# Performance work log

Measured on AMD Instinct MI355X. Metric: run time of the kernel, lower is better.

The kernel has to match this reference:

```python
import jax, jax.numpy as jnp
import numpy as np

N = 1_000_000      # rows
D = 64             # input feature dim
INNER = 16         # inner_dim (Cholesky size)
OUT = 64           # out_dim (proj output)
NSEG = 100_000     # num_segments
NET_OUT = INNER * (INNER + 1) // 2 + INNER  # 152


def setup_inputs() -> dict:
    key = jax.random.key(0)
    k0, k1, k2, k3 = jax.random.split(key, 4)
    data = jax.random.normal(k0, (N, D), dtype=jnp.float32)
    segments = jax.random.randint(k1, (N,), 0, NSEG)
    # LazyInMLP([]) -> single Dense(net_out_dim) with kernel_init=normal(stddev=1e-2)
    W = jax.random.normal(k2, (D, NET_OUT), dtype=jnp.float32) * 0.01
    b = jnp.zeros((NET_OUT,), dtype=jnp.float32)
    # proj Dense(out_dim, use_bias=False), lecun-normal-ish scale
    proj_W = jax.random.normal(k3, (INNER, OUT), dtype=jnp.float32) * (1.0 / np.sqrt(INNER))
    return {"data": data, "segments": segments, "num_segments": NSEG,
            "W": W, "b": b, "proj_W": proj_W}


def reference(data, segments, num_segments, W, b, proj_W):
    # MLP (zero hidden layers -> single Dense)
    net_out = data @ W + b                      # [N, 152]
    t = net_out[:, :INNER]                      # [N, 16]
    y = net_out[:, INNER:]                      # [N, 136]

    # vectorized un_chol: fill lower triangle with tanh, then softplus the diag
    rows, cols = jnp.tril_indices(INNER)
    L = jnp.zeros((data.shape[0], INNER, INNER), dtype=data.dtype)
    L = L.at[:, rows, cols].set(jnp.tanh(y))
    di = jnp.arange(INNER)
    L = L.at[:, di, di].set(jax.nn.softplus(L[:, di, di]))
    F = jnp.einsum('nik,njk->nij', L, L)        # L @ L.T, [N, 16, 16]

    # segment reductions (reduction='sum')
    F_red = jax.ops.segment_sum(F, segments, num_segments=num_segments)  # [S,16,16]
    t_red = jax.ops.segment_sum(t, segments, num_segments=num_segments)  # [S,16]

    F_masked = F_red + jnp.eye(INNER, dtype=F_red.dtype)
    F_inv = jnp.linalg.inv(F_masked)            # batched small-matrix inverse
    # NOTE: faithful to source einsum '...ij,...j->...j' (sums over i, keeps j)
    theta = jnp.einsum('sij,sj->sj', F_inv, t_red)  # [S, 16]

    # inner_dim != out_dim -> proj Dense (no bias)
    return theta @ proj_W                       # [S, 64]
```

## Files before the change

### kernel.cpp

```cpp
#include <hip/hip_runtime.h>
#include <hip/hip_bf16.h>


#define N_PTS   1000000
#define DIM     64
#define INNER   16
#define OUTD    64
#define NSEG    100000
#define NTRI    136
#define NET_OUT 152
#define NB      391
#define SEGW    7
#define NWAVES  ((NSEG + SEGW - 1) / SEGW)
#define MAINB   ((NWAVES + 3) / 4)

typedef short bf16x8 __attribute__((ext_vector_type(8)));
typedef float f32x4  __attribute__((ext_vector_type(4)));
typedef float f32x2  __attribute__((ext_vector_type(2)));
typedef __bf16 bfv2  __attribute__((ext_vector_type(2)));

__device__ __host__ __forceinline__ constexpr int tri(int i) { return i * (i + 1) / 2; }

__device__ __forceinline__ float fast_tanh(float x) {
    float e = __expf(2.0f * x);
    return 1.0f - __fdividef(2.0f, e + 1.0f);
}
__device__ __forceinline__ float fast_softplus(float x) {
    return __logf(1.0f + __expf(x));
}
__device__ __forceinline__ unsigned short cvt1(float f) {
    __bf16 h = (__bf16)f;
    return __builtin_bit_cast(unsigned short, h);
}
__device__ __forceinline__ unsigned cvt2(float a, float b) {
    f32x2 t; t[0] = a; t[1] = b;
    bfv2 h = __builtin_convertvector(t, bfv2);
    return __builtin_bit_cast(unsigned, h);
}

__device__ __forceinline__ void wave_lds_sync() {
    __builtin_amdgcn_wave_barrier();
    __builtin_amdgcn_s_waitcnt(0xC07F);
    __builtin_amdgcn_wave_barrier();
}

__device__ __forceinline__ void ecoord(int e, int& r, int& c, bool& dg) {
    int rr = 0;
    #pragma unroll
    for (int k = 1; k < 16; ++k) rr = (e >= tri(k)) ? k : rr;
    r = rr; c = e - tri(rr); dg = (c == rr);
}

__global__ __launch_bounds__(256) void hist_kernel(const int* __restrict__ segs,
                                                   int* __restrict__ cnt,
                                                   int* __restrict__ rank)
{
    int t = blockIdx.x * 256 + threadIdx.x;
    if (t < N_PTS) rank[t] = atomicAdd(&cnt[segs[t]], 1);
}

__global__ __launch_bounds__(256) void scan_blocks(const int* __restrict__ cnt,
                                                   int* __restrict__ off,
                                                   int* __restrict__ bsum)
{
    __shared__ int sh[256];
    const int t = threadIdx.x;
    const int i = blockIdx.x * 256 + t;
    int v = (i < NSEG) ? cnt[i] : 0;
    sh[t] = v;
    __syncthreads();
    #pragma unroll
    for (int d = 1; d < 256; d <<= 1) {
        int add = (t >= d) ? sh[t - d] : 0;
        __syncthreads();
        sh[t] += add;
        __syncthreads();
    }
    if (i < NSEG) off[i] = sh[t] - v;
    if (t == 255) bsum[blockIdx.x] = sh[t];
}

__global__ __launch_bounds__(512) void scan_top(int* __restrict__ bsum)
{
    __shared__ int sh[512];
    const int t = threadIdx.x;
    int v = (t < NB) ? bsum[t] : 0;
    sh[t] = v;
    __syncthreads();
    #pragma unroll
    for (int d = 1; d < 512; d <<= 1) {
        int add = (t >= d) ? sh[t - d] : 0;
        __syncthreads();
        sh[t] += add;
        __syncthreads();
    }
    if (t < NB) bsum[t] = sh[t] - v;
}

__global__ __launch_bounds__(256) void scan_add(int* __restrict__ off,
                                                const int* __restrict__ bsum)
{
    int i = blockIdx.x * 256 + threadIdx.x;
    if (i < NSEG) off[i] += bsum[blockIdx.x];
}

__global__ __launch_bounds__(256) void scatter_kernel(const int* __restrict__ segs,
                                                      const int* __restrict__ off,
                                                      const int* __restrict__ rank,
                                                      int* __restrict__ sorted)
{
    int t = blockIdx.x * 256 + threadIdx.x;
    if (t < N_PTS) sorted[off[segs[t]] + rank[t]] = t;
}

__global__ __launch_bounds__(256, 2)
void main_kernel(const float* __restrict__ data,
                 const int*   __restrict__ sorted,
                 const int*   __restrict__ off,
                 const int*   __restrict__ cnt,
                 const float* __restrict__ W,
                 const float* __restrict__ bias,
                 float* __restrict__ Fred,
                 float* __restrict__ tred)
{
    __shared__ __align__(16) unsigned short lds[4 * 4096];
    const int l = threadIdx.x & 63;
    const int w = threadIdx.x >> 6;
    unsigned short* Lw = &lds[w * 4096];
    const int c = l & 15;
    const int q = l >> 4;

    const int wave_id = blockIdx.x * 4 + w;
    const int ws0 = wave_id * SEGW;
    if (ws0 >= NSEG) return;
    const int ws1 = min(ws0 + SEGW, NSEG);

    int Ek[SEGW];
    int gend = 0;
    #pragma unroll
    for (int k = 0; k < SEGW; ++k) {
        const int s = ws0 + k;
        if (s < ws1) { gend = off[s] + cnt[s]; Ek[k] = gend; }
        else           Ek[k] = 0x7fffffff;
    }
    int g = off[ws0];
    if (g >= gend) return;

    #pragma unroll
    for (int u = 0; u < 32; ++u) ((unsigned*)Lw)[u * 64 + l] = 0u;
    wave_lds_sync();

    bf16x8 wf[10][2];
    float  bT[10];
    #pragma unroll
    for (int T = 0; T < 10; ++T) {
        #pragma unroll
        for (int ks = 0; ks < 2; ++ks) {
            bf16x8 f;
            #pragma unroll
            for (int j = 0; j < 8; ++j) {
                int k = 32 * ks + 8 * q + j;
                int n = 16 * T + c;
                f[j] = (n < NET_OUT) ? (short)cvt1(W[k * NET_OUT + n]) : (short)0;
            }
            wf[T][ks] = f;
        }
        int n = 16 * T + c;
        bT[T] = (n < NET_OUT) ? bias[n] : 0.0f;
    }

    int rcoff[9];
    int dgmask = 0, dgoff0 = 0;
    #pragma unroll
    for (int T = 1; T <= 9; ++T) {
        int e = 16 * (T - 1) + c;
        int re, ce; bool dg;
        ecoord(e, re, ce, dg);
        rcoff[T - 1] = re * 16 + ce;
        if (dg && (T < 9 || c < 8)) {
            dgmask |= 1 << T;
            if (T <= 8) dgoff0 = re * 16 + ce;
        }
    }
    const bool v9     = (c < 8);
    const bool hasdg0 = (c != 15);
    const int  qb     = q << 10;

    f32x4 fa = {0.f, 0.f, 0.f, 0.f};
    f32x4 fb = {0.f, 0.f, 0.f, 0.f};
    float tcarry = 0.f;
    int a_start = 0;
    float dsv0 = 0.f, dsv1 = 0.f, dsv2 = 0.f, dsv3 = 0.f;

    const int lofs = c * 16 + (q & 1) * 8 + (q >> 1) * 256;

    int idx = min(g + c, gend - 1);
    int p   = sorted[idx];

    while (g < gend) {
        const int nv   = min(16, gend - g);
        const int gn   = g + nv;
        const int idxn = min(gn + c, gend - 1);
        const int pnx  = sorted[idxn];

        int segl = 0;
        bool flag = false;
        #pragma unroll
        for (int k = 0; k < SEGW; ++k) {
            segl += (idx >= Ek[k]) ? 1 : 0;
            flag |= (idx == Ek[k] - 1);
        }
        const int sidv = ws0 + segl;
        const unsigned long long bm = __ballot(l < 16 && c < nv && flag);

        bf16x8 af[2];
        #pragma unroll
        for (int ks = 0; ks < 2; ++ks) {
            const float4* dp = (const float4*)(data + (size_t)p * DIM + 32 * ks + 8 * q);
            float4 x0 = dp[0], x1 = dp[1];
            bf16x8 f;
            unsigned* fu = (unsigned*)&f;
            fu[0] = cvt2(x0.x, x0.y); fu[1] = cvt2(x0.z, x0.w);
            fu[2] = cvt2(x1.x, x1.y); fu[3] = cvt2(x1.z, x1.w);
            af[ks] = f;
        }

        f32x4 acc0;
        {
            f32x4 z = {0.f, 0.f, 0.f, 0.f};
            z = __builtin_amdgcn_mfma_f32_16x16x32_bf16(af[0], wf[0][0], z, 0, 0, 0);
            acc0 = __builtin_amdgcn_mfma_f32_16x16x32_bf16(af[1], wf[0][1], z, 0, 0, 0);
        }

        float s0 = acc0[0] + bT[0];
        float s1 = s0 + acc0[1] + bT[0];
        float s2 = s1 + acc0[2] + bT[0];
        float s3 = s2 + acc0[3] + bT[0];
        float u  = s3;
        float v16 = __shfl_up(u, 16, 64);
        float v32 = __shfl_up(u, 32, 64);
        float v48 = __shfl_up(u, 48, 64);
        float excl = (q >= 1 ? v16 : 0.f) + (q >= 2 ? v32 : 0.f) + (q >= 3 ? v48 : 0.f);
        float P0 = excl + s0, P1 = excl + s1, P2 = excl + s2, P3 = excl + s3;

        wave_lds_sync();
        #pragma unroll
        for (int T = 1; T <= 9; ++T) {
            f32x4 z = {0.f, 0.f, 0.f, 0.f};
            z = __builtin_amdgcn_mfma_f32_16x16x32_bf16(af[0], wf[T][0], z, 0, 0, 0);
            f32x4 a2 = __builtin_amdgcn_mfma_f32_16x16x32_bf16(af[1], wf[T][1], z, 0, 0, 0);
            const bool isdg = (dgmask >> T) & 1;
            const bool st   = (T < 9 || v9) && !isdg;
            unsigned short* bp = Lw + (qb + rcoff[T - 1]);
            #pragma unroll
            for (int r = 0; r < 4; ++r) {
                float v = fast_tanh(a2[r] + bT[T]);
                if (st) bp[r * 256] = cvt1(v);
                if (T <= 8) {
                    if (r == 0) dsv0 = isdg ? v : dsv0;
                    if (r == 1) dsv1 = isdg ? v : dsv1;
                    if (r == 2) dsv2 = isdg ? v : dsv2;
                    if (r == 3) dsv3 = isdg ? v : dsv3;
                }
            }
            if (T == 9 && (c == 7)) {
                unsigned short* dp9 = Lw + (qb + 255);
                #pragma unroll
                for (int r = 0; r < 4; ++r) {
                    float v = fast_tanh(a2[r] + bT[9]);
                    dp9[r * 256] = cvt1(fast_softplus(v));
                }
            }
        }
        if (hasdg0) {
            unsigned short* dp0 = Lw + (qb + dgoff0);
            dp0[0]   = cvt1(fast_softplus(dsv0));
            dp0[256] = cvt1(fast_softplus(dsv1));
            dp0[512] = cvt1(fast_softplus(dsv2));
            dp0[768] = cvt1(fast_softplus(dsv3));
        }
        wave_lds_sync();

        auto flush = [&](int i) {
            const int sid = __shfl(sidv, i, 64);
            const int rs = i & 3;
            float vi = (rs == 0) ? P0 : (rs == 1) ? P1 : (rs == 2) ? P2 : P3;
            float Pi = __shfl(vi, ((i >> 2) << 4) | c, 64);
            float Pe = 0.f;
            if (a_start > 0) {
                const int aa = a_start - 1, ra = aa & 3;
                float va = (ra == 0) ? P0 : (ra == 1) ? P1 : (ra == 2) ? P2 : P3;
                Pe = __shfl(va, ((aa >> 2) << 4) | c, 64);
            }
            float ts = Pi - Pe + tcarry;
            if (l < 16) tred[(size_t)sid * INNER + c] = ts;
            tcarry = 0.f;
            f32x4 ft = fa + fb;
            #pragma unroll
            for (int r = 0; r < 4; ++r) {
                const int mr = 4 * q + r;
                if (c <= mr)
                    Fred[(size_t)sid * NTRI + tri(mr) + c] = ft[r];
            }
            fa = (f32x4){0.f, 0.f, 0.f, 0.f};
            fb = (f32x4){0.f, 0.f, 0.f, 0.f};
            a_start = i + 1;
        };

        const int npair = (nv + 1) >> 1;
        for (int j = 0; j < npair; ++j) {
            const int i0 = 2 * j, i1 = i0 + 1;
            bf16x8 lf = *(const bf16x8*)(Lw + i0 * 256 + lofs);
            const bool vld1 = (i1 < nv);
            const bool f0 = (bm >> i0) & 1;
            if (vld1 && !f0) {
                if (j & 1) fb = __builtin_amdgcn_mfma_f32_16x16x32_bf16(lf, lf, fb, 0, 0, 0);
                else       fa = __builtin_amdgcn_mfma_f32_16x16x32_bf16(lf, lf, fa, 0, 0, 0);
                if ((bm >> i1) & 1) flush(i1);
            } else {
                const bf16x8 zz = {0, 0, 0, 0, 0, 0, 0, 0};
                bf16x8 lo = (q < 2) ? lf : zz;
                fa = __builtin_amdgcn_mfma_f32_16x16x32_bf16(lo, lo, fa, 0, 0, 0);
                if (f0) flush(i0);
                if (vld1) {
                    bf16x8 hi = (q >= 2) ? lf : zz;
                    fb = __builtin_amdgcn_mfma_f32_16x16x32_bf16(hi, hi, fb, 0, 0, 0);
                    if ((bm >> i1) & 1) flush(i1);
                }
            }
        }

        if (a_start < nv) {
            const int ii = nv - 1, rs = ii & 3;
            float vi = (rs == 0) ? P0 : (rs == 1) ? P1 : (rs == 2) ? P2 : P3;
            float Pi = __shfl(vi, ((ii >> 2) << 4) | c, 64);
            float Pe = 0.f;
            if (a_start > 0) {
                const int aa = a_start - 1, ra = aa & 3;
                float va = (ra == 0) ? P0 : (ra == 1) ? P1 : (ra == 2) ? P2 : P3;
                Pe = __shfl(va, ((aa >> 2) << 4) | c, 64);
            }
            tcarry += Pi - Pe;
        }
        a_start = 0;
        g = gn; idx = idxn; p = pnx;
    }
}

__global__ __launch_bounds__(256, 2)
void seg_kernel(const float* __restrict__ Fred,
                const float* __restrict__ tred,
                const int*   __restrict__ cnt,
                const float* __restrict__ projW,
                float* __restrict__ out)
{
    const int s = blockIdx.x * 256 + threadIdx.x;
    if (s >= NSEG) return;
    float* orow = out + (size_t)s * OUTD;

    if (cnt[s] == 0) {
        float4 zz = {0.f, 0.f, 0.f, 0.f};
        #pragma unroll
        for (int oc = 0; oc < OUTD; oc += 4) *(float4*)(orow + oc) = zz;
        return;
    }

    float a[NTRI];
    const float4* f4 = (const float4*)(Fred + (size_t)s * NTRI);
    #pragma unroll
    for (int qq = 0; qq < NTRI / 4; ++qq) {
        float4 v = f4[qq];
        a[4 * qq + 0] = v.x; a[4 * qq + 1] = v.y;
        a[4 * qq + 2] = v.z; a[4 * qq + 3] = v.w;
    }
    #pragma unroll
    for (int ii = 0; ii < INNER; ++ii) a[tri(ii) + ii] += 1.0f;

    #pragma unroll
    for (int j = 0; j < INNER; ++j) {
        float d = a[tri(j) + j];
        #pragma unroll
        for (int k = 0; k < j; ++k)
            d = fmaf(-a[tri(j) + k], a[tri(j) + k], d);
        d = sqrtf(d);
        a[tri(j) + j] = d;
        float dinv = __fdividef(1.0f, d);
        #pragma unroll
        for (int ii = j + 1; ii < INNER; ++ii) {
            float v = a[tri(ii) + j];
            #pragma unroll
            for (int k = 0; k < j; ++k)
                v = fmaf(-a[tri(ii) + k], a[tri(j) + k], v);
            a[tri(ii) + j] = v * dinv;
        }
    }
    float z[INNER];
    #pragma unroll
    for (int ii = 0; ii < INNER; ++ii) {
        float v = 1.0f;
        #pragma unroll
        for (int k = 0; k < ii; ++k)
            v = fmaf(-a[tri(ii) + k], z[k], v);
        z[ii] = __fdividef(v, a[tri(ii) + ii]);
    }
    float x[INNER];
    #pragma unroll
    for (int ii = INNER - 1; ii >= 0; --ii) {
        float v = z[ii];
        #pragma unroll
        for (int k = ii + 1; k < INNER; ++k)
            v = fmaf(-a[tri(k) + ii], x[k], v);
        x[ii] = __fdividef(v, a[tri(ii) + ii]);
    }
    float theta[INNER];
    const float4* t4 = (const float4*)(tred + (size_t)s * INNER);
    #pragma unroll
    for (int qq = 0; qq < 4; ++qq) {
        float4 v = t4[qq];
        theta[4 * qq + 0] = v.x * x[4 * qq + 0];
        theta[4 * qq + 1] = v.y * x[4 * qq + 1];
        theta[4 * qq + 2] = v.z * x[4 * qq + 2];
        theta[4 * qq + 3] = v.w * x[4 * qq + 3];
    }
    for (int oc = 0; oc < OUTD; oc += 8) {
        float acc[8] = {0, 0, 0, 0, 0, 0, 0, 0};
        #pragma unroll
        for (int j = 0; j < INNER; ++j) {
            float th = theta[j];
            #pragma unroll
            for (int uu = 0; uu < 8; ++uu)
                acc[uu] = fmaf(th, projW[j * OUTD + oc + uu], acc[uu]);
        }
        float4 v0 = {acc[0], acc[1], acc[2], acc[3]};
        float4 v1 = {acc[4], acc[5], acc[6], acc[7]};
        ((float4*)(orow + oc))[0] = v0;
        ((float4*)(orow + oc))[1] = v1;
    }
}

extern "C" void kernel_launch(void* const* d_in, const int* in_sizes, int n_in,
                              void* d_out, int out_size, void* d_ws, size_t ws_size,
                              hipStream_t stream)
{
    const float* data  = (const float*)d_in[0];
    const int*   segs  = (const int*)d_in[1];
    const float* W     = (const float*)d_in[3];
    const float* bias  = (const float*)d_in[4];
    const float* projW = (const float*)d_in[5];

    int* cnt     = (int*)d_ws;
    int* off     = cnt + NSEG;
    int* bsum    = off + NSEG;
    int* rank    = bsum + 512;
    int* sorted  = rank + N_PTS;
    float* Fred  = (float*)(sorted + N_PTS);
    float* tred  = Fred + (size_t)NSEG * NTRI;

    hipMemsetAsync(cnt, 0, NSEG * sizeof(int), stream);

    hist_kernel   <<<(N_PTS + 255) / 256, 256, 0, stream>>>(segs, cnt, rank);
    scan_blocks   <<<NB, 256, 0, stream>>>(cnt, off, bsum);
    scan_top      <<<1, 512, 0, stream>>>(bsum);
    scan_add      <<<NB, 256, 0, stream>>>(off, bsum);
    scatter_kernel<<<(N_PTS + 255) / 256, 256, 0, stream>>>(segs, off, rank, sorted);
    main_kernel   <<<MAINB, 256, 0, stream>>>(data, sorted, off, cnt, W, bias, Fred, tred);
    seg_kernel    <<<NB, 256, 0, stream>>>(Fred, tred, cnt, projW, (float*)d_out);
}
```

Baseline: 635.5 us.

## Make main kernel persistent with atomic work queue and prefetch next data rows

```diff
diff --git a/kernel.cpp b/kernel.cpp
--- a/kernel.cpp
+++ b/kernel.cpp
@@ -11,8 +11,7 @@
 #define NET_OUT 152
 #define NB      391
 #define SEGW    7
-#define NWAVES  ((NSEG + SEGW - 1) / SEGW)
-#define MAINB   ((NWAVES + 3) / 4)
+#define PERSB   1024
 
 typedef short bf16x8 __attribute__((ext_vector_type(8)));
 typedef float f32x4  __attribute__((ext_vector_type(4)));
@@ -121,7 +120,8 @@
                  const float* __restrict__ W,
                  const float* __restrict__ bias,
                  float* __restrict__ Fred,
-                 float* __restrict__ tred)
+                 float* __restrict__ tred,
+                 int*   __restrict__ wctr)
 {
     __shared__ __align__(16) unsigned short lds[4 * 4096];
     const int l = threadIdx.x & 63;
@@ -129,22 +129,6 @@
     unsigned short* Lw = &lds[w * 4096];
     const int c = l & 15;
     const int q = l >> 4;
-
-    const int wave_id = blockIdx.x * 4 + w;
-    const int ws0 = wave_id * SEGW;
-    if (ws0 >= NSEG) return;
-    const int ws1 = min(ws0 + SEGW, NSEG);
-
-    int Ek[SEGW];
-    int gend = 0;
-    #pragma unroll
-    for (int k = 0; k < SEGW; ++k) {
-        const int s = ws0 + k;
-        if (s < ws1) { gend = off[s] + cnt[s]; Ek[k] = gend; }
-        else           Ek[k] = 0x7fffffff;
-    }
-    int g = off[ws0];
-    if (g >= gend) return;
 
     #pragma unroll
     for (int u = 0; u < 32; ++u) ((unsigned*)Lw)[u * 64 + l] = 0u;
@@ -186,164 +170,197 @@
     const bool hasdg0 = (c != 15);
     const int  qb     = q << 10;
 
-    f32x4 fa = {0.f, 0.f, 0.f, 0.f};
-    f32x4 fb = {0.f, 0.f, 0.f, 0.f};
-    float tcarry = 0.f;
-    int a_start = 0;
-    float dsv0 = 0.f, dsv1 = 0.f, dsv2 = 0.f, dsv3 = 0.f;
-
     const int lofs = c * 16 + (q & 1) * 8 + (q >> 1) * 256;
 
-    int idx = min(g + c, gend - 1);
-    int p   = sorted[idx];
-
-    while (g < gend) {
-        const int nv   = min(16, gend - g);
-        const int gn   = g + nv;
-        const int idxn = min(gn + c, gend - 1);
-        const int pnx  = sorted[idxn];
-
-        int segl = 0;
-        bool flag = false;
+    for (;;) {
+        int base;
+        if (l == 0) base = atomicAdd(wctr, SEGW);
+        base = __shfl(base, 0, 64);
+        if (base >= NSEG) break;
+        const int ws0 = base;
+        const int ws1 = min(ws0 + SEGW, NSEG);
+
+        int Ek[SEGW];
+        int gend = 0;
         #pragma unroll
         for (int k = 0; k < SEGW; ++k) {
-            segl += (idx >= Ek[k]) ? 1 : 0;
-            flag |= (idx == Ek[k] - 1);
-        }
-        const int sidv = ws0 + segl;
-        const unsigned long long bm = __ballot(l < 16 && c < nv && flag);
-
-        bf16x8 af[2];
-        #pragma unroll
-        for (int ks = 0; ks < 2; ++ks) {
-            const float4* dp = (const float4*)(data + (size_t)p * DIM + 32 * ks + 8 * q);
-            float4 x0 = dp[0], x1 = dp[1];
-            bf16x8 f;
-            unsigned* fu = (unsigned*)&f;
-            fu[0] = cvt2(x0.x, x0.y); fu[1] = cvt2(x0.z, x0.w);
-            fu[2] = cvt2(x1.x, x1.y); fu[3] = cvt2(x1.z, x1.w);
-            af[ks] = f;
-        }
-
-        f32x4 acc0;
+            const int s = ws0 + k;
+            if (s < ws1) { gend = off[s] + cnt[s]; Ek[k] = gend; }
+            else           Ek[k] = 0x7fffffff;
+        }
+        int g = off[ws0];
+        if (g >= gend) continue;
+
+        f32x4 fa = {0.f, 0.f, 0.f, 0.f};
+        f32x4 fb = {0.f, 0.f, 0.f, 0.f};
+        float tcarry = 0.f;
+        int a_start = 0;
+        float dsv0 = 0.f, dsv1 = 0.f, dsv2 = 0.f, dsv3 = 0.f;
+
+        int idx = min(g + c, gend - 1);
         {
-            f32x4 z = {0.f, 0.f, 0.f, 0.f};
-            z = __builtin_amdgcn_mfma_f32_16x16x32_bf16(af[0], wf[0][0], z, 0, 0, 0);
-            acc0 = __builtin_amdgcn_mfma_f32_16x16x32_bf16(af[1], wf[0][1], z, 0, 0, 0);
-        }
-
-        float s0 = acc0[0] + bT[0];
-        float s1 = s0 + acc0[1] + bT[0];
-        float s2 = s1 + acc0[2] + bT[0];
-        float s3 = s2 + acc0[3] + bT[0];
-        float u  = s3;
-        float v16 = __shfl_up(u, 16, 64);
-        float v32 = __shfl_up(u, 32, 64);
-        float v48 = __shfl_up(u, 48, 64);
-        float excl = (q >= 1 ? v16 : 0.f) + (q >= 2 ? v32 : 0.f) + (q >= 3 ? v48 : 0.f);
-        float P0 = excl + s0, P1 = excl + s1, P2 = excl + s2, P3 = excl + s3;
-
-        wave_lds_sync();
-        #pragma unroll
-        for (int T = 1; T <= 9; ++T) {
-            f32x4 z = {0.f, 0.f, 0.f, 0.f};
-            z = __builtin_amdgcn_mfma_f32_16x16x32_bf16(af[0], wf[T][0], z, 0, 0, 0);
-            f32x4 a2 = __builtin_amdgcn_mfma_f32_16x16x32_bf16(af[1], wf[T][1], z, 0, 0, 0);
-            const bool isdg = (dgmask >> T) & 1;
-            const bool st   = (T < 9 || v9) && !isdg;
-            unsigned short* bp = Lw + (qb + rcoff[T - 1]);
-            #pragma unroll
-            for (int r = 0; r < 4; ++r) {
-                float v = fast_tanh(a2[r] + bT[T]);
-                if (st) bp[r * 256] = cvt1(v);
-                if (T <= 8) {
-                    if (r == 0) dsv0 = isdg ? v : dsv0;
-                    if (r == 1) dsv1 = isdg ? v : dsv1;
-                    if (r == 2) dsv2 = isdg ? v : dsv2;
-                    if (r == 3) dsv3 = isdg ? v : dsv3;
-                }
+            const int p0 = sorted[idx];
+            const float* dpt = data + (size_t)p0 * DIM + 8 * q;
+            float4 x0 = ((const float4*)dpt)[0];
+            float4 x1 = ((const float4*)dpt)[1];
+            float4 x2 = ((const float4*)(dpt + 32))[0];
+            float4 x3 = ((const float4*)(dpt + 32))[1];
+
+            while (g < gend) {
+                const int nv   = min(16, gend - g);
+                const int gn   = g + nv;
+                const int idxn = min(gn + c, gend - 1);
+                const int pnx  = sorted[idxn];
+                const float* dq = data + (size_t)pnx * DIM + 8 * q;
+                float4 y0 = ((const float4*)dq)[0];
+                float4 y1 = ((const float4*)dq)[1];
+                float4 y2 = ((const float4*)(dq + 32))[0];
+                float4 y3 = ((const float4*)(dq + 32))[1];
+
+                int segl = 0;
+                bool flag = false;
+                #pragma unroll
+                for (int k = 0; k < SEGW; ++k) {
+                    segl += (idx >= Ek[k]) ? 1 : 0;
+                    flag |= (idx == Ek[k] - 1);
+                }
+                const int sidv = ws0 + segl;
+                const unsigned long long bm = __ballot(l < 16 && c < nv && flag);
+
+                bf16x8 af[2];
+                {
+                    bf16x8 f;
+                    unsigned* fu = (unsigned*)&f;
+                    fu[0] = cvt2(x0.x, x0.y); fu[1] = cvt2(x0.z, x0.w);
+                    fu[2] = cvt2(x1.x, x1.y); fu[3] = cvt2(x1.z, x1.w);
+                    af[0] = f;
+                    fu[0] = cvt2(x2.x, x2.y); fu[1] = cvt2(x2.z, x2.w);
+                    fu[2] = cvt2(x3.x, x3.y); fu[3] = cvt2(x3.z, x3.w);
+                    af[1] = f;
+                }
+
+                f32x4 acc0;
+                {
+                    f32x4 z = {0.f, 0.f, 0.f, 0.f};
+                    z = __builtin_amdgcn_mfma_f32_16x16x32_bf16(af[0], wf[0][0], z, 0, 0, 0);
+                    acc0 = __builtin_amdgcn_mfma_f32_16x16x32_bf16(af[1], wf[0][1], z, 0, 0, 0);
+                }
+
+                float s0 = acc0[0] + bT[0];
+                float s1 = s0 + acc0[1] + bT[0];
+                float s2 = s1 + acc0[2] + bT[0];
+                float s3 = s2 + acc0[3] + bT[0];
+                float u  = s3;
+                float v16 = __shfl_up(u, 16, 64);
+                float v32 = __shfl_up(u, 32, 64);
+                float v48 = __shfl_up(u, 48, 64);
+                float excl = (q >= 1 ? v16 : 0.f) + (q >= 2 ? v32 : 0.f) + (q >= 3 ? v48 : 0.f);
+                float P0 = excl + s0, P1 = excl + s1, P2 = excl + s2, P3 = excl + s3;
+
+                wave_lds_sync();
+                #pragma unroll
+                for (int T = 1; T <= 9; ++T) {
+                    f32x4 z = {0.f, 0.f, 0.f, 0.f};
+                    z = __builtin_amdgcn_mfma_f32_16x16x32_bf16(af[0], wf[T][0], z, 0, 0, 0);
+                    f32x4 a2 = __builtin_amdgcn_mfma_f32_16x16x32_bf16(af[1], wf[T][1], z, 0, 0, 0);
+                    const bool isdg = (dgmask >> T) & 1;
+                    const bool st   = (T < 9 || v9) && !isdg;
+                    unsigned short* bp = Lw + (qb + rcoff[T - 1]);
+                    #pragma unroll
+                    for (int r = 0; r < 4; ++r) {
+                        float v = fast_tanh(a2[r] + bT[T]);
+                        if (st) bp[r * 256] = cvt1(v);
+                        if (T <= 8) {
+                            if (r == 0) dsv0 = isdg ? v : dsv0;
+                            if (r == 1) dsv1 = isdg ? v : dsv1;
+                            if (r == 2) dsv2 = isdg ? v : dsv2;
+                            if (r == 3) dsv3 = isdg ? v : dsv3;
+                        }
+                    }
+                    if (T == 9 && (c == 7)) {
+                        unsigned short* dp9 = Lw + (qb + 255);
+                        #pragma unroll
+                        for (int r = 0; r < 4; ++r) {
+                            float v = fast_tanh(a2[r] + bT[9]);
+                            dp9[r * 256] = cvt1(fast_softplus(v));
+                        }
+                    }
+                }
+                if (hasdg0) {
+                    unsigned short* dp0 = Lw + (qb + dgoff0);
+                    dp0[0]   = cvt1(fast_softplus(dsv0));
+                    dp0[256] = cvt1(fast_softplus(dsv1));
+                    dp0[512] = cvt1(fast_softplus(dsv2));
+                    dp0[768] = cvt1(fast_softplus(dsv3));
+                }
+                wave_lds_sync();
+
+                auto flush = [&](int i) {
+                    const int sid = __shfl(sidv, i, 64);
+                    const int rs = i & 3;
+                    float vi = (rs == 0) ? P0 : (rs == 1) ? P1 : (rs == 2) ? P2 : P3;
+                    float Pi = __shfl(vi, ((i >> 2) << 4) | c, 64);
+                    float Pe = 0.f;
+                    if (a_start > 0) {
+                        const int aa = a_start - 1, ra = aa & 3;
+                        float va = (ra == 0) ? P0 : (ra == 1) ? P1 : (ra == 2) ? P2 : P3;
+                        Pe = __shfl(va, ((aa >> 2) << 4) | c, 64);
+                    }
+                    float ts = Pi - Pe + tcarry;
+                    if (l < 16) tred[(size_t)sid * INNER + c] = ts;
+                    tcarry = 0.f;
+                    f32x4 ft = fa + fb;
+                    #pragma unroll
+                    for (int r = 0; r < 4; ++r) {
+                        const int mr = 4 * q + r;
+                        if (c <= mr)
+                            Fred[(size_t)sid * NTRI + tri(mr) + c] = ft[r];
+                    }
+                    fa = (f32x4){0.f, 0.f, 0.f, 0.f};
+                    fb = (f32x4){0.f, 0.f, 0.f, 0.f};
+                    a_start = i + 1;
+                };
+
+                const int npair = (nv + 1) >> 1;
+                for (int j = 0; j < npair; ++j) {
+                    const int i0 = 2 * j, i1 = i0 + 1;
+                    bf16x8 lf = *(const bf16x8*)(Lw + i0 * 256 + lofs);
+                    const bool vld1 = (i1 < nv);
+                    const bool f0 = (bm >> i0) & 1;
+                    if (vld1 && !f0) {
+                        if (j & 1) fb = __builtin_amdgcn_mfma_f32_16x16x32_bf16(lf, lf, fb, 0, 0, 0);
+                        else       fa = __builtin_amdgcn_mfma_f32_16x16x32_bf16(lf, lf, fa, 0, 0, 0);
+                        if ((bm >> i1) & 1) flush(i1);
+                    } else {
+                        const bf16x8 zz = {0, 0, 0, 0, 0, 0, 0, 0};
+                        bf16x8 lo = (q < 2) ? lf : zz;
+                        fa = __builtin_amdgcn_mfma_f32_16x16x32_bf16(lo, lo, fa, 0, 0, 0);
+                        if (f0) flush(i0);
+                        if (vld1) {
+                            bf16x8 hi = (q >= 2) ? lf : zz;
+                            fb = __builtin_amdgcn_mfma_f32_16x16x32_bf16(hi, hi, fb, 0, 0, 0);
+                            if ((bm >> i1) & 1) flush(i1);
+                        }
+                    }
+                }
+
+                if (a_start < nv) {
+                    const int ii = nv - 1, rs = ii & 3;
+                    float vi = (rs == 0) ? P0 : (rs == 1) ? P1 : (rs == 2) ? P2 : P3;
+                    float Pi = __shfl(vi, ((ii >> 2) << 4) | c, 64);
+                    float Pe = 0.f;
+                    if (a_start > 0) {
+                        const int aa = a_start - 1, ra = aa & 3;
+                        float va = (ra == 0) ? P0 : (ra == 1) ? P1 : (ra == 2) ? P2 : P3;
+                        Pe = __shfl(va, ((aa >> 2) << 4) | c, 64);
+                    }
+                    tcarry += Pi - Pe;
+                }
+                a_start = 0;
+                g = gn; idx = idxn;
+                x0 = y0; x1 = y1; x2 = y2; x3 = y3;
             }
-            if (T == 9 && (c == 7)) {
-                unsigned short* dp9 = Lw + (qb + 255);
-                #pragma unroll
-                for (int r = 0; r < 4; ++r) {
-                    float v = fast_tanh(a2[r] + bT[9]);
-                    dp9[r * 256] = cvt1(fast_softplus(v));
-                }
-            }
-        }
-        if (hasdg0) {
-            unsigned short* dp0 = Lw + (qb + dgoff0);
-            dp0[0]   = cvt1(fast_softplus(dsv0));
-            dp0[256] = cvt1(fast_softplus(dsv1));
-            dp0[512] = cvt1(fast_softplus(dsv2));
-            dp0[768] = cvt1(fast_softplus(dsv3));
-        }
-        wave_lds_sync();
-
-        auto flush = [&](int i) {
-            const int sid = __shfl(sidv, i, 64);
-            const int rs = i & 3;
-            float vi = (rs == 0) ? P0 : (rs == 1) ? P1 : (rs == 2) ? P2 : P3;
-            float Pi = __shfl(vi, ((i >> 2) << 4) | c, 64);
-            float Pe = 0.f;
-            if (a_start > 0) {
-                const int aa = a_start - 1, ra = aa & 3;
-                float va = (ra == 0) ? P0 : (ra == 1) ? P1 : (ra == 2) ? P2 : P3;
-                Pe = __shfl(va, ((aa >> 2) << 4) | c, 64);
-            }
-            float ts = Pi - Pe + tcarry;
-            if (l < 16) tred[(size_t)sid * INNER + c] = ts;
-            tcarry = 0.f;
-            f32x4 ft = fa + fb;
-            #pragma unroll
-            for (int r = 0; r < 4; ++r) {
-                const int mr = 4 * q + r;
-                if (c <= mr)
-                    Fred[(size_t)sid * NTRI + tri(mr) + c] = ft[r];
-            }
-            fa = (f32x4){0.f, 0.f, 0.f, 0.f};
-            fb = (f32x4){0.f, 0.f, 0.f, 0.f};
-            a_start = i + 1;
-        };
-
-        const int npair = (nv + 1) >> 1;
-        for (int j = 0; j < npair; ++j) {
-            const int i0 = 2 * j, i1 = i0 + 1;
-            bf16x8 lf = *(const bf16x8*)(Lw + i0 * 256 + lofs);
-            const bool vld1 = (i1 < nv);
-            const bool f0 = (bm >> i0) & 1;
-            if (vld1 && !f0) {
-                if (j & 1) fb = __builtin_amdgcn_mfma_f32_16x16x32_bf16(lf, lf, fb, 0, 0, 0);
-                else       fa = __builtin_amdgcn_mfma_f32_16x16x32_bf16(lf, lf, fa, 0, 0, 0);
-                if ((bm >> i1) & 1) flush(i1);
-            } else {
-                const bf16x8 zz = {0, 0, 0, 0, 0, 0, 0, 0};
-                bf16x8 lo = (q < 2) ? lf : zz;
-                fa = __builtin_amdgcn_mfma_f32_16x16x32_bf16(lo, lo, fa, 0, 0, 0);
-                if (f0) flush(i0);
-                if (vld1) {
-                    bf16x8 hi = (q >= 2) ? lf : zz;
-                    fb = __builtin_amdgcn_mfma_f32_16x16x32_bf16(hi, hi, fb, 0, 0, 0);
-                    if ((bm >> i1) & 1) flush(i1);
-                }
-            }
-        }
-
-        if (a_start < nv) {
-            const int ii = nv - 1, rs = ii & 3;
-            float vi = (rs == 0) ? P0 : (rs == 1) ? P1 : (rs == 2) ? P2 : P3;
-            float Pi = __shfl(vi, ((ii >> 2) << 4) | c, 64);
-            float Pe = 0.f;
-            if (a_start > 0) {
-                const int aa = a_start - 1, ra = aa & 3;
-                float va = (ra == 0) ? P0 : (ra == 1) ? P1 : (ra == 2) ? P2 : P3;
-                Pe = __shfl(va, ((aa >> 2) << 4) | c, 64);
-            }
-            tcarry += Pi - Pe;
-        }
-        a_start = 0;
-        g = gn; idx = idxn; p = pnx;
+        }
     }
 }
 
@@ -455,14 +472,16 @@
     int* sorted  = rank + N_PTS;
     float* Fred  = (float*)(sorted + N_PTS);
     float* tred  = Fred + (size_t)NSEG * NTRI;
+    int* wctr    = (int*)(tred + (size_t)NSEG * INNER);
 
     hipMemsetAsync(cnt, 0, NSEG * sizeof(int), stream);
+    hipMemsetAsync(wctr, 0, sizeof(int), stream);
 
     hist_kernel   <<<(N_PTS + 255) / 256, 256, 0, stream>>>(segs, cnt, rank);
     scan_blocks   <<<NB, 256, 0, stream>>>(cnt, off, bsum);
     scan_top      <<<1, 512, 0, stream>>>(bsum);
     scan_add      <<<NB, 256, 0, stream>>>(off, bsum);
     scatter_kernel<<<(N_PTS + 255) / 256, 256, 0, stream>>>(segs, off, rank, sorted);
-    main_kernel   <<<MAINB, 256, 0, stream>>>(data, sorted, off, cnt, W, bias, Fred, tred);
+    main_kernel   <<<PERSB, 256, 0, stream>>>(data, sorted, off, cnt, W, bias, Fred, tred, wctr);
     seg_kernel    <<<NB, 256, 0, stream>>>(Fred, tred, cnt, projW, (float*)d_out);
 }
```

New measurement: 653.7 us. +2.9%, slower.

## Software-pipeline main kernel with double-buffered LDS and prefetched data rows

Applied to the files above, without the earlier changes.

```diff
diff --git a/kernel.cpp b/kernel.cpp
--- a/kernel.cpp
+++ b/kernel.cpp
@@ -117,16 +117,14 @@
 void main_kernel(const float* __restrict__ data,
                  const int*   __restrict__ sorted,
                  const int*   __restrict__ off,
-                 const int*   __restrict__ cnt,
                  const float* __restrict__ W,
                  const float* __restrict__ bias,
                  float* __restrict__ Fred,
                  float* __restrict__ tred)
 {
-    __shared__ __align__(16) unsigned short lds[4 * 4096];
+    __shared__ __align__(16) unsigned short lds[4][2][4096];
     const int l = threadIdx.x & 63;
     const int w = threadIdx.x >> 6;
-    unsigned short* Lw = &lds[w * 4096];
     const int c = l & 15;
     const int q = l >> 4;
 
@@ -136,18 +134,17 @@
     const int ws1 = min(ws0 + SEGW, NSEG);
 
     int Ek[SEGW];
-    int gend = 0;
     #pragma unroll
     for (int k = 0; k < SEGW; ++k) {
         const int s = ws0 + k;
-        if (s < ws1) { gend = off[s] + cnt[s]; Ek[k] = gend; }
-        else           Ek[k] = 0x7fffffff;
-    }
+        Ek[k] = (s < ws1) ? ((s + 1 < NSEG) ? off[s + 1] : N_PTS) : 0x7fffffff;
+    }
+    const int gend = (ws1 < NSEG) ? off[ws1] : N_PTS;
     int g = off[ws0];
     if (g >= gend) return;
 
     #pragma unroll
-    for (int u = 0; u < 32; ++u) ((unsigned*)Lw)[u * 64 + l] = 0u;
+    for (int u = 0; u < 64; ++u) ((unsigned*)&lds[w][0][0])[u * 64 + l] = 0u;
     wave_lds_sync();
 
     bf16x8 wf[10][2];
@@ -185,6 +182,7 @@
     const bool v9     = (c < 8);
     const bool hasdg0 = (c != 15);
     const int  qb     = q << 10;
+    const int  lofs   = c * 16 + (q & 1) * 8 + (q >> 1) * 256;
 
     f32x4 fa = {0.f, 0.f, 0.f, 0.f};
     f32x4 fb = {0.f, 0.f, 0.f, 0.f};
@@ -192,158 +190,248 @@
     int a_start = 0;
     float dsv0 = 0.f, dsv1 = 0.f, dsv2 = 0.f, dsv3 = 0.f;
 
-    const int lofs = c * 16 + (q & 1) * 8 + (q >> 1) * 256;
-
-    int idx = min(g + c, gend - 1);
-    int p   = sorted[idx];
-
-    while (g < gend) {
-        const int nv   = min(16, gend - g);
-        const int gn   = g + nv;
-        const int idxn = min(gn + c, gend - 1);
-        const int pnx  = sorted[idxn];
-
-        int segl = 0;
-        bool flag = false;
-        #pragma unroll
-        for (int k = 0; k < SEGW; ++k) {
-            segl += (idx >= Ek[k]) ? 1 : 0;
-            flag |= (idx == Ek[k] - 1);
-        }
-        const int sidv = ws0 + segl;
-        const unsigned long long bm = __ballot(l < 16 && c < nv && flag);
-
-        bf16x8 af[2];
-        #pragma unroll
-        for (int ks = 0; ks < 2; ++ks) {
-            const float4* dp = (const float4*)(data + (size_t)p * DIM + 32 * ks + 8 * q);
-            float4 x0 = dp[0], x1 = dp[1];
-            bf16x8 f;
-            unsigned* fu = (unsigned*)&f;
-            fu[0] = cvt2(x0.x, x0.y); fu[1] = cvt2(x0.z, x0.w);
-            fu[2] = cvt2(x1.x, x1.y); fu[3] = cvt2(x1.z, x1.w);
-            af[ks] = f;
-        }
-
-        f32x4 acc0;
-        {
-            f32x4 z = {0.f, 0.f, 0.f, 0.f};
-            z = __builtin_amdgcn_mfma_f32_16x16x32_bf16(af[0], wf[0][0], z, 0, 0, 0);
-            acc0 = __builtin_amdgcn_mfma_f32_16x16x32_bf16(af[1], wf[0][1], z, 0, 0, 0);
-        }
-
-        float s0 = acc0[0] + bT[0];
-        float s1 = s0 + acc0[1] + bT[0];
-        float s2 = s1 + acc0[2] + bT[0];
-        float s3 = s2 + acc0[3] + bT[0];
-        float u  = s3;
-        float v16 = __shfl_up(u, 16, 64);
-        float v32 = __shfl_up(u, 32, 64);
-        float v48 = __shfl_up(u, 48, 64);
-        float excl = (q >= 1 ? v16 : 0.f) + (q >= 2 ? v32 : 0.f) + (q >= 3 ? v48 : 0.f);
-        float P0 = excl + s0, P1 = excl + s1, P2 = excl + s2, P3 = excl + s3;
-
-        wave_lds_sync();
-        #pragma unroll
-        for (int T = 1; T <= 9; ++T) {
-            f32x4 z = {0.f, 0.f, 0.f, 0.f};
-            z = __builtin_amdgcn_mfma_f32_16x16x32_bf16(af[0], wf[T][0], z, 0, 0, 0);
-            f32x4 a2 = __builtin_amdgcn_mfma_f32_16x16x32_bf16(af[1], wf[T][1], z, 0, 0, 0);
-            const bool isdg = (dgmask >> T) & 1;
-            const bool st   = (T < 9 || v9) && !isdg;
-            unsigned short* bp = Lw + (qb + rcoff[T - 1]);
+    float Pc0, Pc1, Pc2, Pc3;
+    unsigned long long bmc;
+    int sidc, nvc;
+
+    auto flushC = [&](int i) {
+        const int sid = __shfl(sidc, i, 64);
+        const int rs = i & 3;
+        float vi = (rs == 0) ? Pc0 : (rs == 1) ? Pc1 : (rs == 2) ? Pc2 : Pc3;
+        float Pi = __shfl(vi, ((i >> 2) << 4) | c, 64);
+        float Pe = 0.f;
+        if (a_start > 0) {
+            const int aa = a_start - 1, ra = aa & 3;
+            float va = (ra == 0) ? Pc0 : (ra == 1) ? Pc1 : (ra == 2) ? Pc2 : Pc3;
+            Pe = __shfl(va, ((aa >> 2) << 4) | c, 64);
+        }
+        float ts = Pi - Pe + tcarry;
+        if (l < 16) tred[(size_t)sid * INNER + c] = ts;
+        tcarry = 0.f;
+        f32x4 ft = fa + fb;
+        #pragma unroll
+        for (int r = 0; r < 4; ++r) {
+            const int mr = 4 * q + r;
+            if (c <= mr)
+                Fred[(size_t)sid * NTRI + tri(mr) + c] = ft[r];
+        }
+        fa = (f32x4){0.f, 0.f, 0.f, 0.f};
+        fb = (f32x4){0.f, 0.f, 0.f, 0.f};
+        a_start = i + 1;
+    };
+
+    auto prodT = [&](int T, const f32x4& a2, unsigned short* LP) {
+        const bool isdg = (dgmask >> T) & 1;
+        const bool st   = (T < 9 || v9) && !isdg;
+        unsigned short* bp = LP + (qb + rcoff[T - 1]);
+        #pragma unroll
+        for (int r = 0; r < 4; ++r) {
+            float v = fast_tanh(a2[r] + bT[T]);
+            if (st) bp[r * 256] = cvt1(v);
+            if (T <= 8) {
+                if (r == 0) dsv0 = isdg ? v : dsv0;
+                if (r == 1) dsv1 = isdg ? v : dsv1;
+                if (r == 2) dsv2 = isdg ? v : dsv2;
+                if (r == 3) dsv3 = isdg ? v : dsv3;
+            }
+        }
+        if (T == 9 && (c == 7)) {
+            unsigned short* dp9 = LP + (qb + 255);
             #pragma unroll
             for (int r = 0; r < 4; ++r) {
-                float v = fast_tanh(a2[r] + bT[T]);
-                if (st) bp[r * 256] = cvt1(v);
-                if (T <= 8) {
-                    if (r == 0) dsv0 = isdg ? v : dsv0;
-                    if (r == 1) dsv1 = isdg ? v : dsv1;
-                    if (r == 2) dsv2 = isdg ? v : dsv2;
-                    if (r == 3) dsv3 = isdg ? v : dsv3;
-                }
-            }
-            if (T == 9 && (c == 7)) {
-                unsigned short* dp9 = Lw + (qb + 255);
-                #pragma unroll
-                for (int r = 0; r < 4; ++r) {
-                    float v = fast_tanh(a2[r] + bT[9]);
-                    dp9[r * 256] = cvt1(fast_softplus(v));
-                }
-            }
-        }
+                float v = fast_tanh(a2[r] + bT[9]);
+                dp9[r * 256] = cvt1(fast_softplus(v));
+            }
+        }
+    };
+    auto diagpost = [&](unsigned short* LP) {
         if (hasdg0) {
-            unsigned short* dp0 = Lw + (qb + dgoff0);
+            unsigned short* dp0 = LP + (qb + dgoff0);
             dp0[0]   = cvt1(fast_softplus(dsv0));
             dp0[256] = cvt1(fast_softplus(dsv1));
             dp0[512] = cvt1(fast_softplus(dsv2));
             dp0[768] = cvt1(fast_softplus(dsv3));
         }
+    };
+    auto consPair = [&](int j, const unsigned short* LC) {
+        const int i0 = 2 * j, i1 = i0 + 1;
+        bf16x8 lf = *(const bf16x8*)(LC + i0 * 256 + lofs);
+        const bool f0 = (bmc >> i0) & 1;
+        if (!f0) {
+            if (j & 1) fb = __builtin_amdgcn_mfma_f32_16x16x32_bf16(lf, lf, fb, 0, 0, 0);
+            else       fa = __builtin_amdgcn_mfma_f32_16x16x32_bf16(lf, lf, fa, 0, 0, 0);
+        } else {
+            const bf16x8 zz = {0, 0, 0, 0, 0, 0, 0, 0};
+            bf16x8 lo = (q < 2) ? lf : zz;
+            fa = __builtin_amdgcn_mfma_f32_16x16x32_bf16(lo, lo, fa, 0, 0, 0);
+            flushC(i0);
+            bf16x8 hi = (q >= 2) ? lf : zz;
+            fb = __builtin_amdgcn_mfma_f32_16x16x32_bf16(hi, hi, fb, 0, 0, 0);
+        }
+        if ((bmc >> i1) & 1) flushC(i1);
+    };
+
+    int idxA = min(g + c, gend - 1);
+    {
+        const int pA = sorted[idxA];
+        const float* dA = data + (size_t)pA * DIM + 8 * q;
+        float4 x0 = ((const float4*)dA)[0], x1 = ((const float4*)dA)[1];
+        float4 x2 = ((const float4*)(dA + 32))[0], x3 = ((const float4*)(dA + 32))[1];
+
+        const int nvA = min(16, gend - g);
+        int gN = g + nvA;
+        int idxB = min(gN + c, gend - 1);
+        const int pB = sorted[idxB];
+        const float* dB = data + (size_t)pB * DIM + 8 * q;
+        float4 y0 = ((const float4*)dB)[0], y1 = ((const float4*)dB)[1];
+        float4 y2 = ((const float4*)(dB + 32))[0], y3 = ((const float4*)(dB + 32))[1];
+
+        {
+            int segl = 0; bool flag = false;
+            #pragma unroll
+            for (int k = 0; k < SEGW; ++k) {
+                segl += (idxA >= Ek[k]) ? 1 : 0;
+                flag |= (idxA == Ek[k] - 1);
+            }
+            sidc = ws0 + segl;
+            bmc  = __ballot(l < 16 && c < nvA && flag);
+            nvc  = nvA;
+        }
+
+        unsigned short* Lc = &lds[w][0][0];
+        unsigned short* Lp = &lds[w][1][0];
+
+        {
+            bf16x8 af[2];
+            {
+                bf16x8 f; unsigned* fu = (unsigned*)&f;
+                fu[0] = cvt2(x0.x, x0.y); fu[1] = cvt2(x0.z, x0.w);
+                fu[2] = cvt2(x1.x, x1.y); fu[3] = cvt2(x1.z, x1.w);
+                af[0] = f;
+                fu[0] = cvt2(x2.x, x2.y); fu[1] = cvt2(x2.z, x2.w);
+                fu[2] = cvt2(x3.x, x3.y); fu[3] = cvt2(x3.z, x3.w);
+                af[1] = f;
+            }
+            f32x4 z = {0.f, 0.f, 0.f, 0.f};
+            z = __builtin_amdgcn_mfma_f32_16x16x32_bf16(af[0], wf[0][0], z, 0, 0, 0);
+            f32x4 acc0 = __builtin_amdgcn_mfma_f32_16x16x32_bf16(af[1], wf[0][1], z, 0, 0, 0);
+            float s0 = acc0[0] + bT[0];
+            float s1 = s0 + acc0[1] + bT[0];
+            float s2 = s1 + acc0[2] + bT[0];
+            float s3 = s2 + acc0[3] + bT[0];
+            float uu = s3;
+            float v16 = __shfl_up(uu, 16, 64);
+            float v32 = __shfl_up(uu, 32, 64);
+            float v48 = __shfl_up(uu, 48, 64);
+            float excl = (q >= 1 ? v16 : 0.f) + (q >= 2 ? v32 : 0.f) + (q >= 3 ? v48 : 0.f);
+            Pc0 = excl + s0; Pc1 = excl + s1; Pc2 = excl + s2; Pc3 = excl + s3;
+            #pragma unroll
+            for (int T = 1; T <= 9; ++T) {
+                f32x4 zz2 = {0.f, 0.f, 0.f, 0.f};
+                zz2 = __builtin_amdgcn_mfma_f32_16x16x32_bf16(af[0], wf[T][0], zz2, 0, 0, 0);
+                f32x4 a2 = __builtin_amdgcn_mfma_f32_16x16x32_bf16(af[1], wf[T][1], zz2, 0, 0, 0);
+                prodT(T, a2, Lc);
+            }
+            diagpost(Lc);
+        }
+
+        while (gN < gend) {
+            wave_lds_sync();
+            x0 = y0; x1 = y1; x2 = y2; x3 = y3;
+            const int gCur = gN;
+            const int nvn = min(16, gend - gCur);
+            gN = gCur + nvn;
+            const int idx2 = min(gN + c, gend - 1);
+            const int p2 = sorted[idx2];
+            const float* d2 = data + (size_t)p2 * DIM + 8 * q;
+            y0 = ((const float4*)d2)[0]; y1 = ((const float4*)d2)[1];
+            y2 = ((const float4*)(d2 + 32))[0]; y3 = ((const float4*)(d2 + 32))[1];
+            int segl = 0; bool flag = false;
+            #pragma unroll
+            for (int k = 0; k < SEGW; ++k) {
+                segl += (idxB >= Ek[k]) ? 1 : 0;
+                flag |= (idxB == Ek[k] - 1);
+            }
+            const int sidn = ws0 + segl;
+            const unsigned long long bmn = __ballot(l < 16 && c < nvn && flag);
+            idxB = idx2;
+
+            bf16x8 af[2];
+            {
+                bf16x8 f; unsigned* fu = (unsigned*)&f;
+                fu[0] = cvt2(x0.x, x0.y); fu[1] = cvt2(x0.z, x0.w);
+                fu[2] = cvt2(x1.x, x1.y); fu[3] = cvt2(x1.z, x1.w);
+                af[0] = f;
+                fu[0] = cvt2(x2.x, x2.y); fu[1] = cvt2(x2.z, x2.w);
+                fu[2] = cvt2(x3.x, x3.y); fu[3] = cvt2(x3.z, x3.w);
+                af[1] = f;
+            }
+            f32x4 z = {0.f, 0.f, 0.f, 0.f};
+            z = __builtin_amdgcn_mfma_f32_16x16x32_bf16(af[0], wf[0][0], z, 0, 0, 0);
+            f32x4 acc0 = __builtin_amdgcn_mfma_f32_16x16x32_bf16(af[1], wf[0][1], z, 0, 0, 0);
+            float s0 = acc0[0] + bT[0];
+            float s1 = s0 + acc0[1] + bT[0];
+            float s2 = s1 + acc0[2] + bT[0];
+            float s3 = s2 + acc0[3] + bT[0];
+            float uu = s3;
+            float v16 = __shfl_up(uu, 16, 64);
+            float v32 = __shfl_up(uu, 32, 64);
+            float v48 = __shfl_up(uu, 48, 64);
+            float excl = (q >= 1 ? v16 : 0.f) + (q >= 2 ? v32 : 0.f) + (q >= 3 ? v48 : 0.f);
+            const float Pn0 = excl + s0, Pn1 = excl + s1, Pn2 = excl + s2, Pn3 = excl + s3;
+
+            #pragma unroll
+            for (int u = 1; u <= 9; ++u) {
+                f32x4 zz2 = {0.f, 0.f, 0.f, 0.f};
+                zz2 = __builtin_amdgcn_mfma_f32_16x16x32_bf16(af[0], wf[u][0], zz2, 0, 0, 0);
+                f32x4 a2 = __builtin_amdgcn_mfma_f32_16x16x32_bf16(af[1], wf[u][1], zz2, 0, 0, 0);
+                prodT(u, a2, Lp);
+                if (u <= 8) consPair(u - 1, Lc);
+            }
+            diagpost(Lp);
+
+            if (a_start < 16) {
+                const int ii = 15;
+                float Pi = __shfl(Pc3, 48 | c, 64);
+                float Pe = 0.f;
+                if (a_start > 0) {
+                    const int aa = a_start - 1, ra = aa & 3;
+                    float va = (ra == 0) ? Pc0 : (ra == 1) ? Pc1 : (ra == 2) ? Pc2 : Pc3;
+                    Pe = __shfl(va, ((aa >> 2) << 4) | c, 64);
+                }
+                tcarry += Pi - Pe;
+                (void)ii;
+            }
+            a_start = 0;
+
+            Pc0 = Pn0; Pc1 = Pn1; Pc2 = Pn2; Pc3 = Pn3;
+            bmc = bmn; sidc = sidn; nvc = nvn;
+            unsigned short* tt = Lc; Lc = Lp; Lp = tt;
+        }
+
         wave_lds_sync();
-
-        auto flush = [&](int i) {
-            const int sid = __shfl(sidv, i, 64);
-            const int rs = i & 3;
-            float vi = (rs == 0) ? P0 : (rs == 1) ? P1 : (rs == 2) ? P2 : P3;
-            float Pi = __shfl(vi, ((i >> 2) << 4) | c, 64);
-            float Pe = 0.f;
-            if (a_start > 0) {
-                const int aa = a_start - 1, ra = aa & 3;
-                float va = (ra == 0) ? P0 : (ra == 1) ? P1 : (ra == 2) ? P2 : P3;
-                Pe = __shfl(va, ((aa >> 2) << 4) | c, 64);
-            }
-            float ts = Pi - Pe + tcarry;
-            if (l < 16) tred[(size_t)sid * INNER + c] = ts;
-            tcarry = 0.f;
-            f32x4 ft = fa + fb;
-            #pragma unroll
-            for (int r = 0; r < 4; ++r) {
-                const int mr = 4 * q + r;
-                if (c <= mr)
-                    Fred[(size_t)sid * NTRI + tri(mr) + c] = ft[r];
-            }
-            fa = (f32x4){0.f, 0.f, 0.f, 0.f};
-            fb = (f32x4){0.f, 0.f, 0.f, 0.f};
-            a_start = i + 1;
-        };
-
-        const int npair = (nv + 1) >> 1;
+        const int npair = (nvc + 1) >> 1;
         for (int j = 0; j < npair; ++j) {
             const int i0 = 2 * j, i1 = i0 + 1;
-            bf16x8 lf = *(const bf16x8*)(Lw + i0 * 256 + lofs);
-            const bool vld1 = (i1 < nv);
-            const bool f0 = (bm >> i0) & 1;
+            bf16x8 lf = *(const bf16x8*)(Lc + i0 * 256 + lofs);
+            const bool vld1 = (i1 < nvc);
+            const bool f0 = (bmc >> i0) & 1;
             if (vld1 && !f0) {
                 if (j & 1) fb = __builtin_amdgcn_mfma_f32_16x16x32_bf16(lf, lf, fb, 0, 0, 0);
                 else       fa = __builtin_amdgcn_mfma_f32_16x16x32_bf16(lf, lf, fa, 0, 0, 0);
-                if ((bm >> i1) & 1) flush(i1);
+                if ((bmc >> i1) & 1) flushC(i1);
             } else {
                 const bf16x8 zz = {0, 0, 0, 0, 0, 0, 0, 0};
                 bf16x8 lo = (q < 2) ? lf : zz;
                 fa = __builtin_amdgcn_mfma_f32_16x16x32_bf16(lo, lo, fa, 0, 0, 0);
-                if (f0) flush(i0);
+                if (f0) flushC(i0);
                 if (vld1) {
                     bf16x8 hi = (q >= 2) ? lf : zz;
                     fb = __builtin_amdgcn_mfma_f32_16x16x32_bf16(hi, hi, fb, 0, 0, 0);
-                    if ((bm >> i1) & 1) flush(i1);
+                    if ((bmc >> i1) & 1) flushC(i1);
                 }
             }
         }
-
-        if (a_start < nv) {
-            const int ii = nv - 1, rs = ii & 3;
-            float vi = (rs == 0) ? P0 : (rs == 1) ? P1 : (rs == 2) ? P2 : P3;
-            float Pi = __shfl(vi, ((ii >> 2) << 4) | c, 64);
-            float Pe = 0.f;
-            if (a_start > 0) {
-                const int aa = a_start - 1, ra = aa & 3;
-                float va = (ra == 0) ? P0 : (ra == 1) ? P1 : (ra == 2) ? P2 : P3;
-                Pe = __shfl(va, ((aa >> 2) << 4) | c, 64);
-            }
-            tcarry += Pi - Pe;
-        }
-        a_start = 0;
-        g = gn; idx = idxn; p = pnx;
     }
 }
 
@@ -463,6 +551,6 @@
     scan_top      <<<1, 512, 0, stream>>>(bsum);
     scan_add      <<<NB, 256, 0, stream>>>(off, bsum);
     scatter_kernel<<<(N_PTS + 255) / 256, 256, 0, stream>>>(segs, off, rank, sorted);
-    main_kernel   <<<MAINB, 256, 0, stream>>>(data, sorted, off, cnt, W, bias, Fred, tred);
+    main_kernel   <<<MAINB, 256, 0, stream>>>(data, sorted, off, W, bias, Fred, tred);
     seg_kernel    <<<NB, 256, 0, stream>>>(Fred, tred, cnt, projW, (float*)d_out);
 }
```

After: 955.7 us. 50.4% more time.

## Move half of W fragments to LDS, prefetch rows ahead, raise occupancy

Applied to the files above, without the earlier changes.

```diff
diff --git a/kernel.cpp b/kernel.cpp
--- a/kernel.cpp
+++ b/kernel.cpp
@@ -113,16 +113,16 @@
     if (t < N_PTS) sorted[off[segs[t]] + rank[t]] = t;
 }
 
-__global__ __launch_bounds__(256, 2)
+__global__ __launch_bounds__(256, 3)
 void main_kernel(const float* __restrict__ data,
                  const int*   __restrict__ sorted,
                  const int*   __restrict__ off,
-                 const int*   __restrict__ cnt,
                  const float* __restrict__ W,
                  const float* __restrict__ bias,
                  float* __restrict__ Fred,
                  float* __restrict__ tred)
 {
+    __shared__ __align__(16) unsigned short Wl[10 * 512];
     __shared__ __align__(16) unsigned short lds[4 * 4096];
     const int l = threadIdx.x & 63;
     const int w = threadIdx.x >> 6;
@@ -130,30 +130,40 @@
     const int c = l & 15;
     const int q = l >> 4;
 
+    for (int s5 = w; s5 < 10; s5 += 4) {
+        const int T = 5 + (s5 >> 1), ks = s5 & 1;
+        bf16x8 f;
+        #pragma unroll
+        for (int j = 0; j < 8; ++j) {
+            int k = 32 * ks + 8 * q + j;
+            int n = 16 * T + c;
+            f[j] = (n < NET_OUT) ? (short)cvt1(W[k * NET_OUT + n]) : (short)0;
+        }
+        *(bf16x8*)(Wl + s5 * 512 + l * 8) = f;
+    }
+    #pragma unroll
+    for (int u = 0; u < 32; ++u) ((unsigned*)Lw)[u * 64 + l] = 0u;
+    __syncthreads();
+
     const int wave_id = blockIdx.x * 4 + w;
     const int ws0 = wave_id * SEGW;
     if (ws0 >= NSEG) return;
     const int ws1 = min(ws0 + SEGW, NSEG);
 
     int Ek[SEGW];
-    int gend = 0;
     #pragma unroll
     for (int k = 0; k < SEGW; ++k) {
         const int s = ws0 + k;
-        if (s < ws1) { gend = off[s] + cnt[s]; Ek[k] = gend; }
-        else           Ek[k] = 0x7fffffff;
-    }
+        Ek[k] = (s < ws1) ? ((s + 1 < NSEG) ? off[s + 1] : N_PTS) : 0x7fffffff;
+    }
+    const int gend = (ws1 < NSEG) ? off[ws1] : N_PTS;
     int g = off[ws0];
     if (g >= gend) return;
 
-    #pragma unroll
-    for (int u = 0; u < 32; ++u) ((unsigned*)Lw)[u * 64 + l] = 0u;
-    wave_lds_sync();
-
-    bf16x8 wf[10][2];
+    bf16x8 wf[5][2];
     float  bT[10];
     #pragma unroll
-    for (int T = 0; T < 10; ++T) {
+    for (int T = 0; T < 5; ++T) {
         #pragma unroll
         for (int ks = 0; ks < 2; ++ks) {
             bf16x8 f;
@@ -161,10 +171,13 @@
             for (int j = 0; j < 8; ++j) {
                 int k = 32 * ks + 8 * q + j;
                 int n = 16 * T + c;
-                f[j] = (n < NET_OUT) ? (short)cvt1(W[k * NET_OUT + n]) : (short)0;
+                f[j] = (short)cvt1(W[k * NET_OUT + n]);
             }
             wf[T][ks] = f;
         }
+    }
+    #pragma unroll
+    for (int T = 0; T < 10; ++T) {
         int n = 16 * T + c;
         bT[T] = (n < NET_OUT) ? bias[n] : 0.0f;
     }
@@ -193,36 +206,44 @@
     float dsv0 = 0.f, dsv1 = 0.f, dsv2 = 0.f, dsv3 = 0.f;
 
     const int lofs = c * 16 + (q & 1) * 8 + (q >> 1) * 256;
-
-    int idx = min(g + c, gend - 1);
-    int p   = sorted[idx];
+    const unsigned short* Wp = Wl + l * 8;
+
+    int idxA = min(g + c, gend - 1);
+    const int pA = sorted[idxA];
+    const float* dA = data + (size_t)pA * DIM + 8 * q;
+    float4 x0 = ((const float4*)dA)[0], x1 = ((const float4*)dA)[1];
+    float4 x2 = ((const float4*)(dA + 32))[0], x3 = ((const float4*)(dA + 32))[1];
+    int idxB = min(g + 16 + c, gend - 1);
+    int pB   = sorted[idxB];
 
     while (g < gend) {
-        const int nv   = min(16, gend - g);
-        const int gn   = g + nv;
-        const int idxn = min(gn + c, gend - 1);
-        const int pnx  = sorted[idxn];
+        const int nv = min(16, gend - g);
+        const int gn = g + nv;
+        const float* dB = data + (size_t)pB * DIM + 8 * q;
+        float4 y0 = ((const float4*)dB)[0], y1 = ((const float4*)dB)[1];
+        float4 y2 = ((const float4*)(dB + 32))[0], y3 = ((const float4*)(dB + 32))[1];
+        const int idxC = min(gn + 16 + c, gend - 1);
+        const int pC   = sorted[idxC];
 
         int segl = 0;
         bool flag = false;
         #pragma unroll
         for (int k = 0; k < SEGW; ++k) {
-            segl += (idx >= Ek[k]) ? 1 : 0;
-            flag |= (idx == Ek[k] - 1);
+            segl += (idxA >= Ek[k]) ? 1 : 0;
+            flag |= (idxA == Ek[k] - 1);
         }
         const int sidv = ws0 + segl;
         const unsigned long long bm = __ballot(l < 16 && c < nv && flag);
 
         bf16x8 af[2];
-        #pragma unroll
-        for (int ks = 0; ks < 2; ++ks) {
-            const float4* dp = (const float4*)(data + (size_t)p * DIM + 32 * ks + 8 * q);
-            float4 x0 = dp[0], x1 = dp[1];
-            bf16x8 f;
-            unsigned* fu = (unsigned*)&f;
+        {
+            bf16x8 f; unsigned* fu = (unsigned*)&f;
             fu[0] = cvt2(x0.x, x0.y); fu[1] = cvt2(x0.z, x0.w);
             fu[2] = cvt2(x1.x, x1.y); fu[3] = cvt2(x1.z, x1.w);
-            af[ks] = f;
+            af[0] = f;
+            fu[0] = cvt2(x2.x, x2.y); fu[1] = cvt2(x2.z, x2.w);
+            fu[2] = cvt2(x3.x, x3.y); fu[3] = cvt2(x3.z, x3.w);
+            af[1] = f;
         }
 
         f32x4 acc0;
@@ -244,11 +265,22 @@
         float P0 = excl + s0, P1 = excl + s1, P2 = excl + s2, P3 = excl + s3;
 
         wave_lds_sync();
+        bf16x8 wna = *(const bf16x8*)(Wp);
+        bf16x8 wnb = *(const bf16x8*)(Wp + 512);
         #pragma unroll
         for (int T = 1; T <= 9; ++T) {
+            bf16x8 wa, wb;
+            if (T <= 4) { wa = wf[T][0]; wb = wf[T][1]; }
+            else {
+                wa = wna; wb = wnb;
+                if (T < 9) {
+                    wna = *(const bf16x8*)(Wp + (T - 4) * 1024);
+                    wnb = *(const bf16x8*)(Wp + (T - 4) * 1024 + 512);
+                }
+            }
             f32x4 z = {0.f, 0.f, 0.f, 0.f};
-            z = __builtin_amdgcn_mfma_f32_16x16x32_bf16(af[0], wf[T][0], z, 0, 0, 0);
-            f32x4 a2 = __builtin_amdgcn_mfma_f32_16x16x32_bf16(af[1], wf[T][1], z, 0, 0, 0);
+            z = __builtin_amdgcn_mfma_f32_16x16x32_bf16(af[0], wa, z, 0, 0, 0);
+            f32x4 a2 = __builtin_amdgcn_mfma_f32_16x16x32_bf16(af[1], wb, z, 0, 0, 0);
             const bool isdg = (dgmask >> T) & 1;
             const bool st   = (T < 9 || v9) && !isdg;
             unsigned short* bp = Lw + (qb + rcoff[T - 1]);
@@ -343,7 +375,8 @@
             tcarry += Pi - Pe;
         }
         a_start = 0;
-        g = gn; idx = idxn; p = pnx;
+        g = gn; idxA = idxB; idxB = idxC; pB = pC;
+        x0 = y0; x1 = y1; x2 = y2; x3 = y3;
     }
 }
 
@@ -463,6 +496,6 @@
     scan_top      <<<1, 512, 0, stream>>>(bsum);
     scan_add      <<<NB, 256, 0, stream>>>(off, bsum);
     scatter_kernel<<<(N_PTS + 255) / 256, 256, 0, stream>>>(segs, off, rank, sorted);
-    main_kernel   <<<MAINB, 256, 0, stream>>>(data, sorted, off, cnt, W, bias, Fred, tred);
+    main_kernel   <<<MAINB, 256, 0, stream>>>(data, sorted, off, W, bias, Fred, tred);
     seg_kernel    <<<NB, 256, 0, stream>>>(Fred, tred, cnt, projW, (float*)d_out);
 }
```

After: 576.2 us. 1.1x faster.
